# Optimization experiments

Measured on AMD Instinct MI355X. Metric: run time of the kernel, lower is better.

Reference implementation:

```python
import jax, jax.numpy as jnp
import numpy as np


def setup_inputs() -> dict:
    key = jax.random.key(0)
    k_w, k_xi, k_u = jax.random.split(key, 3)
    N, d, M, L, B = 4096, 512, 256, 16, 1024
    W = 2 * L + 1  # window width = 33
    # xavier-normal-ish scale for weight (fan_in=d, fan_out=M*W per torch xavier on last dim pairs)
    w_scale = (2.0 / (W + d)) ** 0.5
    xi_scale = (2.0 / (M + N + 2 * L)) ** 0.5
    weight = jax.random.normal(k_w, (M, W, d), dtype=jnp.float32) * w_scale
    bias = jnp.zeros((M, W, 1), dtype=jnp.float32)
    xi = jax.random.normal(k_xi, (M, N + 2 * L), dtype=jnp.float32) * xi_scale
    u = jax.random.normal(k_u, (B, d), dtype=jnp.float32)
    return {"u": u, "weight": weight, "bias": bias, "xi": xi}


def reference(u, weight, bias, xi):
    # weight: [M, W, d], bias: [M, W, 1], xi: [M, N + W - 1], u: [B, d]
    M, W, d = weight.shape
    N = xi.shape[1] - (W - 1)
    # first_step: G[m, j, b] = sigmoid(sum_k weight[m,j,k] * u[b,k] + bias[m,j])
    G = jax.nn.sigmoid(jnp.einsum('mjd,bd->mjb', weight, u) + bias)  # [M, W, B]
    # im2col-style unfold of xi into overlapping windows, replacing the N-step Python loop
    idx = jnp.arange(N)[:, None] + jnp.arange(W)[None, :]  # [N, W]
    Xw = xi[:, idx]  # [M, N, W]
    # out[n, b] = sum_{m, j} xi[m, n+j] * G[m, j, b]  == torch.cat of iter_prod rows
    return jnp.einsum('mnj,mjb->nb', Xw, G)  # [N, B]
```

## Files before the change

### kernel.cpp

```cpp
#include <hip/hip_runtime.h>
#include <hip/hip_bf16.h>

typedef __attribute__((ext_vector_type(8))) short bf16x8;
typedef __attribute__((ext_vector_type(4))) float f32x4;
typedef unsigned int u32;
typedef unsigned short u16;

#define XI_ROW 4128
#define KP     8448
#define NB     1024
#define NN     4096
#define DDIM   512

__device__ __forceinline__ u16 f2bf(float f) {
  union { float f; unsigned u; } c; c.f = f;
  return (u16)((c.u + 0x7FFFu + ((c.u >> 16) & 1u)) >> 16);
}
__device__ __forceinline__ float bf2f(u16 h) {
  union { u32 u; float f; } c; c.u = ((u32)h) << 16; return c.f;
}
__device__ __forceinline__ u32 pk2bf(float a, float b) {
  return (u32)f2bf(a) | ((u32)f2bf(b) << 16);
}
__device__ __forceinline__ void gld16(const u16* g, u16* l) {
  __builtin_amdgcn_global_load_lds(
      (const __attribute__((address_space(1))) u32*)(const void*)g,
      (__attribute__((address_space(3))) u32*)(void*)l, 16, 0, 0);
}

#define BAR() __builtin_amdgcn_s_barrier()
#define LGKM0() asm volatile("s_waitcnt lgkmcnt(0)" ::: "memory")
#define WAITVM(N) asm volatile("s_waitcnt vmcnt(" #N ")" ::: "memory")
#define SCHED0() __builtin_amdgcn_sched_barrier(0)

__global__ __launch_bounds__(256) void k_prep(
    const float* __restrict__ w, const float* __restrict__ u,
    const float* __restrict__ xi, u16* __restrict__ Wbf,
    u16* __restrict__ Ubf, u16* __restrict__ xiT) {
  __shared__ u16 tile[32][33];
  const int bx = blockIdx.x, t = threadIdx.x;
  if (bx < 4224) {
    int kp = bx * 2 + (t >> 7), tl = t & 127;
    int m = kp & 255, j = kp >> 8;
    float4 v = ((const float4*)(w + (size_t)(m * 33 + j) * DDIM))[tl];
    ((uint2*)(Wbf + (size_t)kp * DDIM))[tl] =
        make_uint2(pk2bf(v.x, v.y), pk2bf(v.z, v.w));
  } else if (bx < 4736) {
    int b = (bx - 4224) * 2 + (t >> 7), tl = t & 127;
    float4 v = ((const float4*)(u + (size_t)b * DDIM))[tl];
    ((uint2*)(Ubf + (size_t)b * DDIM))[tl] =
        make_uint2(pk2bf(v.x, v.y), pk2bf(v.z, v.w));
  } else {
    int bx2 = bx - 4736;
    int cblk = bx2 % 129, mblk = bx2 / 129;
    int c0 = cblk * 32, m0 = mblk * 32;
    int tx = t & 31, ty = t >> 5;
#pragma unroll
    for (int i = 0; i < 4; ++i)
      tile[ty + i * 8][tx] = f2bf(xi[(size_t)(m0 + ty + i * 8) * XI_ROW + c0 + tx]);
    __syncthreads();
#pragma unroll
    for (int i = 0; i < 4; ++i)
      xiT[(size_t)(c0 + ty + i * 8) * 256 + m0 + tx] = tile[tx][ty + i * 8];
  }
}

template<int KSTEPS, int AS, int BS>
__device__ __forceinline__ void gemm_pipeline(
    const u16* __restrict__ aSrc, const u16* __restrict__ bSrc,
    u16* As0, u16* As1, u16* Bl0, u16* Bl1,
    int wid, int wr, int wc, int rl, int kg, int rl7,
    f32x4 (&acc)[4][4]) {

  auto stage = [&](u16* Ab, u16* Bb, int kk) {
#pragma unroll
    for (int i = 0; i < 4; ++i)
      gld16(aSrc + (size_t)i * 8 * AS + kk, &Ab[(wid * 4 + i) * 512]);
#pragma unroll
    for (int i = 0; i < 4; ++i)
      gld16(bSrc + (size_t)i * 8 * BS + kk, &Bb[(wid * 4 + i) * 512]);
  };
  auto compute = [&](const u16* Ab, const u16* Bb) {
#pragma unroll
    for (int kh = 0; kh < 2; ++kh) {
      bf16x8 af[4], bfv[4];
#pragma unroll
      for (int fm = 0; fm < 4; ++fm)
        af[fm] = *(const bf16x8*)&Ab[(wr * 64 + fm * 16 + rl) * 64 +
                                     (((kh * 4 + kg) ^ rl7) * 8)];
#pragma unroll
      for (int fn = 0; fn < 4; ++fn)
        bfv[fn] = *(const bf16x8*)&Bb[(wc * 64 + fn * 16 + rl) * 64 +
                                      (((kh * 4 + kg) ^ rl7) * 8)];
      __builtin_amdgcn_s_setprio(1);
#pragma unroll
      for (int fm = 0; fm < 4; ++fm)
#pragma unroll
        for (int fn = 0; fn < 4; ++fn)
          acc[fm][fn] = __builtin_amdgcn_mfma_f32_16x16x32_bf16(
              af[fm], bfv[fn], acc[fm][fn], 0, 0, 0);
      __builtin_amdgcn_s_setprio(0);
    }
  };

  stage(As0, Bl0, 0);
  WAITVM(0);
  BAR();
#pragma unroll 1
  for (int ts = 0; ts < KSTEPS - 2; ts += 2) {
    stage(As1, Bl1, (ts + 1) * 64);
    WAITVM(8);
    BAR();
    compute(As0, Bl0);
    BAR();
    stage(As0, Bl0, (ts + 2) * 64);
    WAITVM(8);
    BAR();
    compute(As1, Bl1);
    BAR();
  }
  stage(As1, Bl1, (KSTEPS - 1) * 64);
  WAITVM(8);
  BAR();
  compute(As0, Bl0);
  BAR();
  WAITVM(0);
  BAR();
  compute(As1, Bl1);
}

__global__ __launch_bounds__(256) void k_gemm1(
    const u16* __restrict__ Wbf, const u16* __restrict__ Ubf,
    const float* __restrict__ Bsrc, u16* __restrict__ Gt) {
  __shared__ u16 As0[8192], As1[8192], Bl0[8192], Bl1[8192];
  const int r0 = blockIdx.x * 128;
  const int b0 = blockIdx.y * 128;
  const int t = threadIdx.x, lane = t & 63, wid = t >> 6;
  const int wr = wid >> 1, wc = wid & 1;
  const int rl = lane & 15, kg = lane >> 4, rl7 = rl & 7;
  const int lr = lane >> 3, lc = (lane & 7) ^ (lr & 7);
  const u16* aSrc = Wbf + (size_t)(r0 + wid * 32 + lr) * DDIM + lc * 8;
  const u16* bSrc = Ubf + (size_t)(b0 + wid * 32 + lr) * DDIM + lc * 8;

  f32x4 acc[4][4] = {};
  gemm_pipeline<8, DDIM, DDIM>(aSrc, bSrc, As0, As1, Bl0, Bl1,
                               wid, wr, wc, rl, kg, rl7, acc);

#pragma unroll
  for (int fm = 0; fm < 4; ++fm) {
    int kbase = r0 + wr * 64 + fm * 16 + kg * 4;
    float b4[4];
#pragma unroll
    for (int r = 0; r < 4; ++r) {
      int kk = kbase + r;
      b4[r] = Bsrc[(kk & 255) * 33 + (kk >> 8)];
    }
#pragma unroll
    for (int fn = 0; fn < 4; ++fn) {
      int b = b0 + wc * 64 + fn * 16 + rl;
      u16 o[4];
#pragma unroll
      for (int r = 0; r < 4; ++r) {
        float x = acc[fm][fn][r] + b4[r];
        o[r] = f2bf(1.0f / (1.0f + __expf(-x)));
      }
      u16* dst = Gt + (size_t)b * KP + kbase;
      *(u32*)(dst)     = (u32)o[0] | ((u32)o[1] << 16);
      *(u32*)(dst + 2) = (u32)o[2] | ((u32)o[3] << 16);
    }
  }
}

__global__ __launch_bounds__(512, 2) void k_gemm2(
    const u16* __restrict__ xiT, const u16* __restrict__ Gt,
    float* __restrict__ Out, u16* __restrict__ Part, int allbf) {
  __shared__ u16 lds[65536];
  const int lid = blockIdx.x;
  const int b0 = (lid & 3) * 256;
  const int ks = (lid >> 2) & 3;
  const int n0 = (lid >> 4) * 256;
  const int kOff = (ks < 2) ? ks * 2176 : 4352 + (ks - 2) * 2048;
  const int nt = (ks < 2) ? 34 : 32;

  const int t = threadIdx.x, lane = t & 63, wid = t >> 6;
  const int wr = wid >> 2, wc = wid & 3;
  const int rl = lane & 15, kg = lane >> 4, rl7 = rl & 7;
  const int sr = lane >> 3;
  const int sc = (lane & 7) ^ sr;

  const u16* aS = xiT + (size_t)(n0 + wid * 16 + sr) * 256 + kOff + sc * 8;
  const u16* bS = Gt  + (size_t)(b0 + wid * 16 + sr) * KP  + kOff + sc * 8;

  f32x4 acc[8][4] = {};
  bf16x8 af[8], b01[4], b23[4];

  auto stA = [&](int tile, int half, int buf) {
    u16* d = lds + (buf * 4 + half) * 8192 + wid * 1024;
    const u16* s = aS + (size_t)half * 32768 + (size_t)tile * 64;
    gld16(s, d);
    gld16(s + 2048, d + 512);
  };
  auto stB = [&](int tile, int half, int buf) {
    u16* d = lds + (buf * 4 + 2 + half) * 8192 + wid * 1024;
    const u16* s = bS + (size_t)half * 128 * KP + (size_t)tile * 64;
    gld16(s, d);
    gld16(s + (size_t)8 * KP, d + 512);
  };
  auto rdA = [&](int buf, int sub) {
    const u16* p = lds + (buf * 4 + wr) * 8192;
#pragma unroll
    for (int q = 0; q < 4; ++q)
#pragma unroll
      for (int kh = 0; kh < 2; ++kh)
        af[q * 2 + kh] = *(const bf16x8*)
            &p[((sub * 4 + q) * 16 + rl) * 64 + (((kh * 4 + kg) ^ rl7) * 8)];
  };
  auto rdB = [&](int buf, int sub, bf16x8 (&bq)[4]) {
    const u16* p = lds + (buf * 4 + 2 + (wc >> 1)) * 8192;
#pragma unroll
    for (int q = 0; q < 2; ++q)
#pragma unroll
      for (int kh = 0; kh < 2; ++kh)
        bq[q * 2 + kh] = *(const bf16x8*)
            &p[((wc & 1) * 64 + (sub * 2 + q) * 16 + rl) * 64 +
               (((kh * 4 + kg) ^ rl7) * 8)];
  };
  auto mm = [&](int sm, int sn, bf16x8 (&bq)[4]) {
    __builtin_amdgcn_s_setprio(1);
#pragma unroll
    for (int q = 0; q < 4; ++q)
#pragma unroll
      for (int p = 0; p < 2; ++p)
#pragma unroll
        for (int kh = 0; kh < 2; ++kh)
          acc[sm * 4 + q][sn * 2 + p] = __builtin_amdgcn_mfma_f32_16x16x32_bf16(
              af[q * 2 + kh], bq[p * 2 + kh], acc[sm * 4 + q][sn * 2 + p], 0, 0, 0);
    __builtin_amdgcn_s_setprio(0);
  };

  auto runIter = [&](int T, bool s2) {
    rdA(0, 0); rdB(0, 0, b01); stA(T + 1, 0, 1);
    SCHED0(); BAR(); LGKM0(); SCHED0(); mm(0, 0, b01); BAR();
    rdB(0, 1, b23); stA(T + 1, 1, 1);
    SCHED0(); BAR(); LGKM0(); SCHED0(); mm(0, 1, b23); BAR();
    rdA(0, 1); if (s2) stB(T + 2, 0, 0);
    SCHED0(); BAR(); LGKM0(); SCHED0(); mm(1, 0, b01); BAR();
    if (s2) { stB(T + 2, 1, 0); WAITVM(4); } else { WAITVM(0); }
    SCHED0(); BAR(); SCHED0(); mm(1, 1, b23); BAR();
    rdA(1, 0); rdB(1, 0, b01); if (s2) stA(T + 2, 0, 0);
    SCHED0(); BAR(); LGKM0(); SCHED0(); mm(0, 0, b01); BAR();
    rdB(1, 1, b23); if (s2) stA(T + 2, 1, 0);
    SCHED0(); BAR(); LGKM0(); SCHED0(); mm(0, 1, b23); BAR();
    rdA(1, 1); if (s2) stB(T + 3, 0, 1);
    SCHED0(); BAR(); LGKM0(); SCHED0(); mm(1, 0, b01); BAR();
    if (s2) { stB(T + 3, 1, 1); WAITVM(4); }
    SCHED0(); BAR(); SCHED0(); mm(1, 1, b23); BAR();
  };

  stA(0, 0, 0); stA(0, 1, 0); stB(0, 0, 0); stB(0, 1, 0);
  stB(1, 0, 1); stB(1, 1, 1);
  WAITVM(4);
  BAR();

  const int nIter = nt >> 1;
#pragma unroll 1
  for (int it = 0; it < nIter - 1; ++it) runIter(it * 2, true);
  runIter((nIter - 1) * 2, false);

  if (!allbf && ks == 0) {
#pragma unroll
    for (int fm = 0; fm < 8; ++fm)
#pragma unroll
      for (int fn = 0; fn < 4; ++fn) {
        int n = n0 + wr * 128 + fm * 16 + kg * 4;
        int b = b0 + wc * 64 + fn * 16 + rl;
#pragma unroll
        for (int r = 0; r < 4; ++r)
          Out[(size_t)(n + r) * NB + b] = acc[fm][fn][r];
      }
  } else {
    int slot = allbf ? ks : (ks - 1);
    u16* P = Part + (size_t)slot * (NN * NB);
#pragma unroll
    for (int fm = 0; fm < 8; ++fm)
#pragma unroll
      for (int fn = 0; fn < 4; ++fn) {
        int n = n0 + wr * 128 + fm * 16 + kg * 4;
        int b = b0 + wc * 64 + fn * 16 + rl;
#pragma unroll
        for (int r = 0; r < 4; ++r)
          P[(size_t)(n + r) * NB + b] = f2bf(acc[fm][fn][r]);
      }
  }
}

__global__ __launch_bounds__(256) void k_reduce(float* __restrict__ Out,
                                                const u16* __restrict__ Part,
                                                int allbf) {
  size_t i = (size_t)blockIdx.x * 256 + threadIdx.x;
  float4 a;
  int np;
  if (allbf) { a = make_float4(0.f, 0.f, 0.f, 0.f); np = 4; }
  else       { a = ((const float4*)Out)[i];          np = 3; }
  for (int p = 0; p < np; ++p) {
    ushort4 v = ((const ushort4*)(Part + (size_t)p * (NN * NB)))[i];
    a.x += bf2f(v.x); a.y += bf2f(v.y); a.z += bf2f(v.z); a.w += bf2f(v.w);
  }
  ((float4*)Out)[i] = a;
}

extern "C" void kernel_launch(void* const* d_in, const int* in_sizes, int n_in,
                              void* d_out, int out_size, void* d_ws, size_t ws_size,
                              hipStream_t stream) {
  const float* u  = (const float*)d_in[0];
  const float* w  = (const float*)d_in[1];
  const float* bs = (const float*)d_in[2];
  const float* xi = (const float*)d_in[3];
  float* out = (float*)d_out;

  u16* xiT  = (u16*)d_ws;
  u16* Gt   = (u16*)((char*)d_ws + 2113536);
  u16* Wbf  = (u16*)((char*)d_ws + 19415040);
  u16* Ubf  = (u16*)((char*)d_ws + 28065792);
  u16* Part = (u16*)((char*)d_ws + 19415040);
  const int allbf = (ws_size >= 52969472ull) ? 1 : 0;

  k_prep<<<5768, 256, 0, stream>>>(w, u, xi, Wbf, Ubf, xiT);
  k_gemm1<<<dim3(66, 8), 256, 0, stream>>>(Wbf, Ubf, bs, Gt);
  k_gemm2<<<256, 512, 0, stream>>>(xiT, Gt, out, Part, allbf);
  k_reduce<<<4096, 256, 0, stream>>>(out, Part, allbf);
}
```

Baseline: 103.9 us.

## Reorder global-to-LDS prefetch schedule and drop trailing barriers after MFMA phases

Restructures the software-pipelined main loop so that B-tile prefetches are staggered differently across the eight MFMA phases, and each phase no longer ends with a barrier after its MFMA block. The prologue issues one fewer B stage up front, and vmcnt waits are tightened to match the new in-flight count. The aim is to cut the number of workgroup barriers and overlap more memory traffic with matrix math. The risk is LDS hazards if the reduced synchronisation leaves a buffer being overwritten while another wave still reads it.

```diff
diff --git a/kernel.cpp b/kernel.cpp
--- a/kernel.cpp
+++ b/kernel.cpp
@@ -238,34 +238,35 @@
     __builtin_amdgcn_s_setprio(0);
   };
 
-  auto runIter = [&](int T, bool s2) {
-    rdA(0, 0); rdB(0, 0, b01); stA(T + 1, 0, 1);
-    SCHED0(); BAR(); LGKM0(); SCHED0(); mm(0, 0, b01); BAR();
-    rdB(0, 1, b23); stA(T + 1, 1, 1);
-    SCHED0(); BAR(); LGKM0(); SCHED0(); mm(0, 1, b23); BAR();
-    rdA(0, 1); if (s2) stB(T + 2, 0, 0);
-    SCHED0(); BAR(); LGKM0(); SCHED0(); mm(1, 0, b01); BAR();
-    if (s2) { stB(T + 2, 1, 0); WAITVM(4); } else { WAITVM(0); }
-    SCHED0(); BAR(); SCHED0(); mm(1, 1, b23); BAR();
-    rdA(1, 0); rdB(1, 0, b01); if (s2) stA(T + 2, 0, 0);
-    SCHED0(); BAR(); LGKM0(); SCHED0(); mm(0, 0, b01); BAR();
-    rdB(1, 1, b23); if (s2) stA(T + 2, 1, 0);
-    SCHED0(); BAR(); LGKM0(); SCHED0(); mm(0, 1, b23); BAR();
-    rdA(1, 1); if (s2) stB(T + 3, 0, 1);
-    SCHED0(); BAR(); LGKM0(); SCHED0(); mm(1, 0, b01); BAR();
-    if (s2) { stB(T + 3, 1, 1); WAITVM(4); }
-    SCHED0(); BAR(); SCHED0(); mm(1, 1, b23); BAR();
+  auto runIter = [&](int T, bool s2, bool s3) {
+    rdA(0, 0); rdB(0, 0, b01); stB(T + 1, 1, 1);
+    SCHED0(); BAR(); LGKM0(); SCHED0(); mm(0, 0, b01);
+    rdB(0, 1, b23); stA(T + 1, 0, 1);
+    SCHED0(); BAR(); LGKM0(); SCHED0(); mm(0, 1, b23);
+    rdA(0, 1); stA(T + 1, 1, 1);
+    SCHED0(); BAR(); LGKM0(); SCHED0(); mm(1, 0, b01);
+    if (s2) { stB(T + 2, 0, 0); WAITVM(2); } else { WAITVM(0); }
+    SCHED0(); BAR(); SCHED0(); mm(1, 1, b23);
+    rdA(1, 0); rdB(1, 0, b01); if (s2) stB(T + 2, 1, 0);
+    SCHED0(); BAR(); LGKM0(); SCHED0(); mm(0, 0, b01);
+    rdB(1, 1, b23); if (s2) stA(T + 2, 0, 0);
+    SCHED0(); BAR(); LGKM0(); SCHED0(); mm(0, 1, b23);
+    rdA(1, 1); if (s2) stA(T + 2, 1, 0);
+    SCHED0(); BAR(); LGKM0(); SCHED0(); mm(1, 0, b01);
+    if (s3) { stB(T + 3, 0, 1); WAITVM(2); }
+    else if (s2) { WAITVM(0); }
+    SCHED0(); BAR(); SCHED0(); mm(1, 1, b23);
   };
 
   stA(0, 0, 0); stA(0, 1, 0); stB(0, 0, 0); stB(0, 1, 0);
-  stB(1, 0, 1); stB(1, 1, 1);
-  WAITVM(4);
+  stB(1, 0, 1);
+  WAITVM(2);
   BAR();
 
   const int nIter = nt >> 1;
 #pragma unroll 1
-  for (int it = 0; it < nIter - 1; ++it) runIter(it * 2, true);
-  runIter((nIter - 1) * 2, false);
+  for (int it = 0; it < nIter - 1; ++it) runIter(it * 2, true, true);
+  runIter((nIter - 1) * 2, false, false);
 
   if (!allbf && ks == 0) {
 #pragma unroll
```

Measured after the change: 100.7 us. 3.0% less time.
